# Optimization experiments

Measured on AMD Instinct MI355X. Metric: run time of the kernel, lower is better.

## Reference

```python
import jax, jax.numpy as jnp
import numpy as np

HEADS = 8
C_HEAD = 64  # head dim == in_dim of x
P0, P1 = 2, 3  # adaptive pool output


def setup_inputs() -> dict:
    key = jax.random.key(0)
    ks = jax.random.split(key, 8)
    b, c, h, w = 16, 64, 64, 96
    m, d = 6, 192
    inner = HEADS * C_HEAD  # 512
    return {
        "x": jax.random.normal(ks[0], (b, c, h, w), dtype=jnp.float32),
        "z": jax.random.normal(ks[1], (b, m, d), dtype=jnp.float32),
        "conv_w": jax.random.normal(ks[2], (192, c), dtype=jnp.float32) * 0.02,
        "conv_b": jax.random.normal(ks[3], (192,), dtype=jnp.float32) * 0.02,
        "wq": jax.random.normal(ks[4], (d, inner), dtype=jnp.float32) * 0.02,
        "bq": jax.random.normal(ks[5], (inner,), dtype=jnp.float32) * 0.02,
        "wo": jax.random.normal(ks[6], (inner, d), dtype=jnp.float32) * 0.02,
        "bo": jax.random.normal(ks[7], (d,), dtype=jnp.float32) * 0.02,
    }


def reference(x, z, conv_w, conv_b, wq, bq, wo, bo):
    b, c, h, w = x.shape
    _, m, d = z.shape
    # 1x1 conv (pointwise GEMM over channels) + bias
    xp = jnp.einsum('bchw,oc->bohw', x, conv_w) + conv_b[None, :, None, None]
    # AdaptiveAvgPool2d((2,3)) with exact divisibility -> block mean
    xp = xp.reshape(b, 192, P0, h // P0, P1, w // P1).mean(axis=(3, 5))  # [b,192,2,3]
    # view(b, d, m) then permute(0,2,1) -> [b, m, d]
    z = z + xp.reshape(b, d, m).transpose(0, 2, 1)
    # k = v: view(b, h*w, c), repeat heads along last dim, view(b, heads, h*w, c)
    # (row-major reshape reproduces torch .view semantics exactly)
    kv = jnp.tile(x.reshape(b, h * w, c), (1, 1, HEADS)).reshape(b, HEADS, h * w, C_HEAD)
    # q = Linear(dim, heads*c) then view(b, heads, m, c)
    q = (z @ wq + bq).reshape(b, HEADS, m, C_HEAD)
    scale = C_HEAD ** -0.5
    dots = jnp.einsum('bhmc,bhlc->bhml', q, kv) * scale  # [b,h,m,l]
    attn = jax.nn.softmax(dots, axis=-1)
    out = jnp.einsum('bhml,bhlc->bhmc', attn, kv)
    out = out.transpose(0, 2, 1, 3).reshape(b, m, HEADS * C_HEAD)  # b m (h c)
    return z + out @ wo + bo
```

## Files before the change

### kernel.cpp

```cpp
#include <hip/hip_runtime.h>

#define NB 16
#define NC 64
#define NM 6
#define ND 192
#define NHEADS 8
#define NCH 64
#define NINNER 512
#define PLANE 6144
#define XB (NC*PLANE)
#define NKEY 768
#define NCHUNK 8
#define CK 96

__global__ __launch_bounds__(256) void pool_kernel(const float* __restrict__ x,
                                                   float* __restrict__ xmean) {
    int bc = blockIdx.x;
    const float4* p = (const float4*)(x + (size_t)bc * PLANE);
    int tid = threadIdx.x;
    float acc[6] = {0.f,0.f,0.f,0.f,0.f,0.f};
    #pragma unroll
    for (int k = 0; k < 6; ++k) {
        int idx4 = tid + k * 256;
        int hh = idx4 / 24;
        int w4 = idx4 - hh * 24;
        int j = (hh >> 5) * 3 + (w4 >> 3);
        float4 v = p[idx4];
        acc[j] += v.x + v.y + v.z + v.w;
    }
    int lane = tid & 63, wave = tid >> 6;
    #pragma unroll
    for (int j = 0; j < 6; ++j) {
        float v = acc[j];
        for (int off = 32; off > 0; off >>= 1) v += __shfl_down(v, off, 64);
        acc[j] = v;
    }
    __shared__ float part[4][6];
    if (lane == 0) {
        #pragma unroll
        for (int j = 0; j < 6; ++j) part[wave][j] = acc[j];
    }
    __syncthreads();
    if (tid < 6) {
        float s = part[0][tid] + part[1][tid] + part[2][tid] + part[3][tid];
        xmean[bc * 6 + tid] = s * (1.0f / 1024.0f);
    }
}

__global__ __launch_bounds__(256) void zq_kernel(const float* __restrict__ z,
                                                 const float* __restrict__ conv_w,
                                                 const float* __restrict__ conv_b,
                                                 const float* __restrict__ wq,
                                                 const float* __restrict__ bq,
                                                 const float* __restrict__ xmean,
                                                 float* __restrict__ znew,
                                                 float* __restrict__ qr) {
    int blk = blockIdx.x;
    int cgrp = blk & 7, bm = blk >> 3;
    int b = bm / NM, m = bm - b * NM;
    int tid = threadIdx.x;
    __shared__ float xm[NC];
    __shared__ float zn[ND];
    __shared__ float qpart[3][64];
    if (tid < NC) xm[tid] = xmean[(b * NC + tid) * NM + m];
    __syncthreads();
    if (tid < ND) {
        float a = conv_b[tid];
        const float4* wr4 = (const float4*)(conv_w + tid * NC);
        #pragma unroll
        for (int c4 = 0; c4 < 16; ++c4) {
            float4 w = wr4[c4];
            a += w.x * xm[c4 * 4 + 0] + w.y * xm[c4 * 4 + 1]
               + w.z * xm[c4 * 4 + 2] + w.w * xm[c4 * 4 + 3];
        }
        float v = z[bm * ND + tid] + a;
        zn[tid] = v;
        if (cgrp == 0) znew[bm * ND + tid] = v;
    }
    __syncthreads();
    int colL = tid & 63, ks = tid >> 6;
    int col = cgrp * 64 + colL;
    float a = (ks == 0) ? bq[col] : 0.f;
    int d0 = ks * 48;
    #pragma unroll
    for (int d = d0; d < d0 + 48; ++d) a += zn[d] * wq[d * NINNER + col];
    if (ks > 0) qpart[ks - 1][colL] = a;
    __syncthreads();
    if (ks == 0) {
        float tot = a + qpart[0][colL] + qpart[1][colL] + qpart[2][colL];
        int t = m * 8 + cgrp;
        qr[b * (48 * 64) + t * 64 + colL] = tot;
    }
}

__global__ __launch_bounds__(256, 5) void fattn_kernel(const float* __restrict__ x,
                                                       const float* __restrict__ qr,
                                                       float* __restrict__ po,
                                                       float* __restrict__ ps) {
    int blk = blockIdx.x;
    int chunk = blk & 7, bh = blk >> 3;
    int head = bh & 7, b = bh >> 3;
    int tid = threadIdx.x;
    __shared__ float k_lds[CK][NCH];
    __shared__ float q_lds[NM][NCH];
    __shared__ float s_lds[NM][CK];
    const float* kbase = x + (size_t)b * XB + (size_t)(head * NKEY + chunk * CK) * NCH;

    for (int i = tid; i < NM * NCH; i += 256) {
        int mi = i >> 6, ch = i & 63;
        q_lds[mi][ch] = qr[b * (48 * 64) + (head * NM + mi) * 64 + ch];
    }
    const float4* k4 = (const float4*)kbase;
    #pragma unroll
    for (int r = 0; r < 6; ++r) {
        int i = tid + r * 256;
        int row = i >> 4, c4 = i & 15;
        float4 v = k4[i];
        *(float4*)&k_lds[row][c4 * 4] = v;
    }
    __syncthreads();

    if (tid < 96) {
        int u = tid;
        float a[NM] = {0.f,0.f,0.f,0.f,0.f,0.f};
        #pragma unroll
        for (int c4 = 0; c4 < 16; ++c4) {
            int cc = ((c4 + u) & 15) * 4;
            float4 kv = *(const float4*)&k_lds[u][cc];
            #pragma unroll
            for (int mo = 0; mo < NM; ++mo) {
                float4 qv = *(const float4*)&q_lds[mo][cc];
                a[mo] += kv.x*qv.x + kv.y*qv.y + kv.z*qv.z + kv.w*qv.w;
            }
        }
        #pragma unroll
        for (int mo = 0; mo < NM; ++mo) s_lds[mo][u] = __expf(a[mo] * 0.125f);
    }
    __syncthreads();

    int lane = tid & 63, wave = tid >> 6;

    if (wave < 2) {
        int ch = lane, m0 = wave * 3;
        float a0 = 0.f, a1 = 0.f, a2 = 0.f;
        #pragma unroll
        for (int u0 = 0; u0 < CK; u0 += 4) {
            float4 s0 = *(const float4*)&s_lds[m0 + 0][u0];
            float4 s1 = *(const float4*)&s_lds[m0 + 1][u0];
            float4 s2 = *(const float4*)&s_lds[m0 + 2][u0];
            float kv0 = k_lds[u0 + 0][ch];
            float kv1 = k_lds[u0 + 1][ch];
            float kv2 = k_lds[u0 + 2][ch];
            float kv3 = k_lds[u0 + 3][ch];
            a0 += s0.x*kv0 + s0.y*kv1 + s0.z*kv2 + s0.w*kv3;
            a1 += s1.x*kv0 + s1.y*kv1 + s1.z*kv2 + s1.w*kv3;
            a2 += s2.x*kv0 + s2.y*kv1 + s2.z*kv2 + s2.w*kv3;
        }
        float* pob = po + (size_t)blk * (NM * NCH);
        pob[(m0 + 0) * NCH + ch] = a0;
        pob[(m0 + 1) * NCH + ch] = a1;
        pob[(m0 + 2) * NCH + ch] = a2;
    } else {
        #pragma unroll
        for (int rnd = 0; rnd < 3; ++rnd) {
            int mi = rnd * 2 + (wave - 2);
            float v = s_lds[mi][lane] + ((lane < 32) ? s_lds[mi][64 + lane] : 0.f);
            for (int msk = 1; msk < 64; msk <<= 1) v += __shfl_xor(v, msk, 64);
            if (lane == 0) ps[blk * NM + mi] = v;
        }
    }
}

__global__ __launch_bounds__(256) void proj_kernel(const float* __restrict__ znew,
                                                   const float* __restrict__ po,
                                                   const float* __restrict__ ps,
                                                   const float* __restrict__ wo,
                                                   const float* __restrict__ bo,
                                                   float* __restrict__ out) {
    int blk = blockIdx.x;
    int cgrp = blk & 3, bm = blk >> 2;
    int b = bm / NM, m = bm - b * NM;
    int tid = threadIdx.x;
    __shared__ float4 orow4[128];
    __shared__ float4 part4[16][12];

    if (tid < 128) {
        int h = tid >> 4, c16 = tid & 15;
        int base = (b * NHEADS + h) * NCHUNK;
        const float4* po4 = (const float4*)po;
        float4 n = make_float4(0.f, 0.f, 0.f, 0.f);
        float den = 0.f;
        #pragma unroll
        for (int c = 0; c < NCHUNK; ++c) {
            float4 v = po4[(size_t)(base + c) * 96 + m * 16 + c16];
            n.x += v.x; n.y += v.y; n.z += v.z; n.w += v.w;
            den += ps[(base + c) * NM + m];
        }
        float inv = 1.0f / den;
        n.x *= inv; n.y *= inv; n.z *= inv; n.w *= inv;
        orow4[tid] = n;
    }
    __syncthreads();

    if (tid < 192) {
        int g4 = tid % 12, ks = tid / 12;
        int cb = cgrp * 12 + g4;
        const float4* wo4 = (const float4*)wo;
        const float* orow = (const float*)orow4;
        float4 acc = make_float4(0.f, 0.f, 0.f, 0.f);
        int i0 = ks * 32;
        #pragma unroll 8
        for (int i = i0; i < i0 + 32; ++i) {
            float s = orow[i];
            float4 w = wo4[i * 48 + cb];
            acc.x += s * w.x; acc.y += s * w.y; acc.z += s * w.z; acc.w += s * w.w;
        }
        part4[ks][g4] = acc;
    }
    __syncthreads();

    if (tid < 48) {
        int g4 = tid >> 2, j = tid & 3;
        float s = 0.f;
        #pragma unroll
        for (int ks = 0; ks < 16; ++ks) s += ((const float*)&part4[ks][g4])[j];
        int col = cgrp * 48 + tid;
        out[bm * ND + col] = s + bo[col] + znew[bm * ND + col];
    }
}

extern "C" void kernel_launch(void* const* d_in, const int* in_sizes, int n_in,
                              void* d_out, int out_size, void* d_ws, size_t ws_size,
                              hipStream_t stream) {
    const float* x      = (const float*)d_in[0];
    const float* z      = (const float*)d_in[1];
    const float* conv_w = (const float*)d_in[2];
    const float* conv_b = (const float*)d_in[3];
    const float* wq     = (const float*)d_in[4];
    const float* bq     = (const float*)d_in[5];
    const float* wo     = (const float*)d_in[6];
    const float* bo     = (const float*)d_in[7];
    float* out = (float*)d_out;

    float* ws    = (float*)d_ws;
    float* xmean = ws;
    float* znew  = ws + 6144;
    float* qr    = ws + 24576;
    float* po    = ws + 73728;
    float* ps    = ws + 466944;

    pool_kernel<<<NB*NC, 256, 0, stream>>>(x, xmean);
    zq_kernel<<<NB*NM*8, 256, 0, stream>>>(z, conv_w, conv_b, wq, bq, xmean, znew, qr);
    fattn_kernel<<<NB*NHEADS*NCHUNK, 256, 0, stream>>>(x, qr, po, ps);
    proj_kernel<<<NB*NM*4, 256, 0, stream>>>(znew, po, ps, wo, bo, out);
}
```

Measured before the change: 31.36 us.

## Split q projection algebraically so pooling and z-projection run in one launch

The q projection is split using linearity. The part from z+conv_b and the precomputed product conv_w^T·wq are computed in the same launch as the pooling, in independent block ranges. The remaining xmean·(conv_w^T wq) term is added inside the attention kernel, and proj recomputes znew from conv_w and xmean. This removes one kernel launch and the serial dependency between pooling and the q GEMM. In exchange, every attention block now does redundant 64-length dot products, and floating-point summation order changes.

```diff
diff --git a/kernel.cpp b/kernel.cpp
--- a/kernel.cpp
+++ b/kernel.cpp
@@ -13,90 +13,88 @@
 #define NCHUNK 8
 #define CK 96
 
-__global__ __launch_bounds__(256) void pool_kernel(const float* __restrict__ x,
-                                                   float* __restrict__ xmean) {
-    int bc = blockIdx.x;
-    const float4* p = (const float4*)(x + (size_t)bc * PLANE);
+__global__ __launch_bounds__(256) void k1_kernel(
+    const float* __restrict__ x, const float* __restrict__ z,
+    const float* __restrict__ conv_w, const float* __restrict__ conv_b,
+    const float* __restrict__ wq, const float* __restrict__ bq,
+    float* __restrict__ xmean, float* __restrict__ qz,
+    float* __restrict__ cwt)
+{
+    int bid = blockIdx.x;
     int tid = threadIdx.x;
-    float acc[6] = {0.f,0.f,0.f,0.f,0.f,0.f};
-    #pragma unroll
-    for (int k = 0; k < 6; ++k) {
-        int idx4 = tid + k * 256;
-        int hh = idx4 / 24;
-        int w4 = idx4 - hh * 24;
-        int j = (hh >> 5) * 3 + (w4 >> 3);
-        float4 v = p[idx4];
-        acc[j] += v.x + v.y + v.z + v.w;
-    }
-    int lane = tid & 63, wave = tid >> 6;
-    #pragma unroll
-    for (int j = 0; j < 6; ++j) {
-        float v = acc[j];
-        for (int off = 32; off > 0; off >>= 1) v += __shfl_down(v, off, 64);
-        acc[j] = v;
-    }
-    __shared__ float part[4][6];
-    if (lane == 0) {
-        #pragma unroll
-        for (int j = 0; j < 6; ++j) part[wave][j] = acc[j];
-    }
-    __syncthreads();
-    if (tid < 6) {
-        float s = part[0][tid] + part[1][tid] + part[2][tid] + part[3][tid];
-        xmean[bc * 6 + tid] = s * (1.0f / 1024.0f);
-    }
-}
-
-__global__ __launch_bounds__(256) void zq_kernel(const float* __restrict__ z,
-                                                 const float* __restrict__ conv_w,
-                                                 const float* __restrict__ conv_b,
-                                                 const float* __restrict__ wq,
-                                                 const float* __restrict__ bq,
-                                                 const float* __restrict__ xmean,
-                                                 float* __restrict__ znew,
-                                                 float* __restrict__ qr) {
-    int blk = blockIdx.x;
-    int cgrp = blk & 7, bm = blk >> 3;
-    int b = bm / NM, m = bm - b * NM;
-    int tid = threadIdx.x;
-    __shared__ float xm[NC];
-    __shared__ float zn[ND];
-    __shared__ float qpart[3][64];
-    if (tid < NC) xm[tid] = xmean[(b * NC + tid) * NM + m];
-    __syncthreads();
-    if (tid < ND) {
-        float a = conv_b[tid];
-        const float4* wr4 = (const float4*)(conv_w + tid * NC);
-        #pragma unroll
-        for (int c4 = 0; c4 < 16; ++c4) {
-            float4 w = wr4[c4];
-            a += w.x * xm[c4 * 4 + 0] + w.y * xm[c4 * 4 + 1]
-               + w.z * xm[c4 * 4 + 2] + w.w * xm[c4 * 4 + 3];
-        }
-        float v = z[bm * ND + tid] + a;
-        zn[tid] = v;
-        if (cgrp == 0) znew[bm * ND + tid] = v;
-    }
-    __syncthreads();
-    int colL = tid & 63, ks = tid >> 6;
-    int col = cgrp * 64 + colL;
-    float a = (ks == 0) ? bq[col] : 0.f;
-    int d0 = ks * 48;
-    #pragma unroll
-    for (int d = d0; d < d0 + 48; ++d) a += zn[d] * wq[d * NINNER + col];
-    if (ks > 0) qpart[ks - 1][colL] = a;
-    __syncthreads();
-    if (ks == 0) {
-        float tot = a + qpart[0][colL] + qpart[1][colL] + qpart[2][colL];
-        int t = m * 8 + cgrp;
-        qr[b * (48 * 64) + t * 64 + colL] = tot;
-    }
-}
-
-__global__ __launch_bounds__(256, 5) void fattn_kernel(const float* __restrict__ x,
-                                                       const float* __restrict__ qr,
-                                                       float* __restrict__ po,
-                                                       float* __restrict__ ps) {
+    __shared__ float sh[448];
+
+    if (bid < 1024) {
+        int bc = bid;
+        const float4* p = (const float4*)(x + (size_t)bc * PLANE);
+        float acc[6] = {0.f,0.f,0.f,0.f,0.f,0.f};
+        #pragma unroll
+        for (int k = 0; k < 6; ++k) {
+            int idx4 = tid + k * 256;
+            int hh = idx4 / 24;
+            int w4 = idx4 - hh * 24;
+            int j = (hh >> 5) * 3 + (w4 >> 3);
+            float4 v = p[idx4];
+            acc[j] += v.x + v.y + v.z + v.w;
+        }
+        int lane = tid & 63, wave = tid >> 6;
+        #pragma unroll
+        for (int j = 0; j < 6; ++j) {
+            float v = acc[j];
+            for (int off = 32; off > 0; off >>= 1) v += __shfl_down(v, off, 64);
+            acc[j] = v;
+        }
+        float* part = sh;
+        if (lane == 0) {
+            #pragma unroll
+            for (int j = 0; j < 6; ++j) part[wave * 6 + j] = acc[j];
+        }
+        __syncthreads();
+        if (tid < 6) {
+            float s = part[tid] + part[6 + tid] + part[12 + tid] + part[18 + tid];
+            xmean[bc * 6 + tid] = s * (1.0f / 1024.0f);
+        }
+    } else if (bid < 1792) {
+        int blk = bid - 1024;
+        int cgrp = blk & 7, bm = blk >> 3;
+        float* zc    = sh;
+        float* qpart = sh + 192;
+        if (tid < ND) zc[tid] = z[bm * ND + tid] + conv_b[tid];
+        __syncthreads();
+        int colL = tid & 63, ks = tid >> 6;
+        int col = cgrp * 64 + colL;
+        float a = (ks == 0) ? bq[col] : 0.f;
+        int d0 = ks * 48;
+        #pragma unroll
+        for (int d = d0; d < d0 + 48; ++d) a += zc[d] * wq[d * NINNER + col];
+        if (ks > 0) qpart[(ks - 1) * 64 + colL] = a;
+        __syncthreads();
+        if (ks == 0) {
+            qz[blk * 64 + colL] = a + qpart[colL] + qpart[64 + colL] + qpart[128 + colL];
+        }
+    } else {
+        int j = bid - 1792;
+        int c = tid & 63, cl0 = tid >> 6;
+        float a0 = 0.f, a1 = 0.f;
+        const float* wc = conv_w + c;
+        const float* w0 = wq + j * 8 + cl0;
+        const float* w1 = w0 + 4;
+        #pragma unroll 8
+        for (int d = 0; d < ND; ++d) {
+            float cwv = wc[d * NC];
+            a0 += cwv * w0[d * NINNER];
+            a1 += cwv * w1[d * NINNER];
+        }
+        cwt[(j * 8 + cl0    ) * 64 + c] = a0;
+        cwt[(j * 8 + cl0 + 4) * 64 + c] = a1;
+    }
+}
+
+__global__ __launch_bounds__(256, 5) void fattn_kernel(
+    const float* __restrict__ x, const float* __restrict__ qz,
+    const float* __restrict__ cwt, const float* __restrict__ xmean,
+    float* __restrict__ po, float* __restrict__ ps)
+{
     int blk = blockIdx.x;
     int chunk = blk & 7, bh = blk >> 3;
     int head = bh & 7, b = bh >> 3;
@@ -104,11 +102,12 @@
     __shared__ float k_lds[CK][NCH];
     __shared__ float q_lds[NM][NCH];
     __shared__ float s_lds[NM][CK];
+    __shared__ float xmT[NM][NC];
     const float* kbase = x + (size_t)b * XB + (size_t)(head * NKEY + chunk * CK) * NCH;
 
-    for (int i = tid; i < NM * NCH; i += 256) {
-        int mi = i >> 6, ch = i & 63;
-        q_lds[mi][ch] = qr[b * (48 * 64) + (head * NM + mi) * 64 + ch];
+    for (int i = tid; i < NC * NM; i += 256) {
+        int c = i / 6, m = i - c * 6;
+        xmT[m][c] = xmean[b * 384 + i];
     }
     const float4* k4 = (const float4*)kbase;
     #pragma unroll
@@ -117,6 +116,23 @@
         int row = i >> 4, c4 = i & 15;
         float4 v = k4[i];
         *(float4*)&k_lds[row][c4 * 4] = v;
+    }
+    __syncthreads();
+
+    for (int idx = tid; idx < NM * NCH; idx += 256) {
+        int mi = idx >> 6, ch = idx & 63;
+        int t = head * 6 + mi;
+        int mr = t >> 3;
+        int col = ((t & 7) << 6) | ch;
+        float a = qz[b * 3072 + t * 64 + ch];
+        const float4* cw4 = (const float4*)(cwt + col * 64);
+        const float4* xv4 = (const float4*)&xmT[mr][0];
+        #pragma unroll
+        for (int c4 = 0; c4 < 16; ++c4) {
+            float4 w = cw4[c4], v = xv4[c4];
+            a += w.x*v.x + w.y*v.y + w.z*v.z + w.w*v.w;
+        }
+        q_lds[mi][ch] = a;
     }
     __syncthreads();
 
@@ -139,7 +155,6 @@
     __syncthreads();
 
     int lane = tid & 63, wave = tid >> 6;
-
     if (wave < 2) {
         int ch = lane, m0 = wave * 3;
         float a0 = 0.f, a1 = 0.f, a2 = 0.f;
@@ -171,18 +186,22 @@
     }
 }
 
-__global__ __launch_bounds__(256) void proj_kernel(const float* __restrict__ znew,
-                                                   const float* __restrict__ po,
-                                                   const float* __restrict__ ps,
-                                                   const float* __restrict__ wo,
-                                                   const float* __restrict__ bo,
-                                                   float* __restrict__ out) {
+__global__ __launch_bounds__(256) void proj_kernel(
+    const float* __restrict__ z, const float* __restrict__ conv_w,
+    const float* __restrict__ conv_b, const float* __restrict__ xmean,
+    const float* __restrict__ po, const float* __restrict__ ps,
+    const float* __restrict__ wo, const float* __restrict__ bo,
+    float* __restrict__ out)
+{
     int blk = blockIdx.x;
     int cgrp = blk & 3, bm = blk >> 2;
     int b = bm / NM, m = bm - b * NM;
     int tid = threadIdx.x;
     __shared__ float4 orow4[128];
     __shared__ float4 part4[16][12];
+    __shared__ float xmc[NC];
+
+    if (tid < NC) xmc[tid] = xmean[b * 384 + tid * 6 + m];
 
     if (tid < 128) {
         int h = tid >> 4, c16 = tid & 15;
@@ -220,12 +239,20 @@
     __syncthreads();
 
     if (tid < 48) {
-        int g4 = tid >> 2, j = tid & 3;
+        int g4 = tid >> 2, jj = tid & 3;
         float s = 0.f;
         #pragma unroll
-        for (int ks = 0; ks < 16; ++ks) s += ((const float*)&part4[ks][g4])[j];
+        for (int ks = 0; ks < 16; ++ks) s += ((const float*)&part4[ks][g4])[jj];
         int col = cgrp * 48 + tid;
-        out[bm * ND + col] = s + bo[col] + znew[bm * ND + col];
+        float zn = z[bm * ND + col] + conv_b[col];
+        const float4* cw4 = (const float4*)(conv_w + col * NC);
+        const float4* xv4 = (const float4*)xmc;
+        #pragma unroll
+        for (int c4 = 0; c4 < 16; ++c4) {
+            float4 w = cw4[c4], v = xv4[c4];
+            zn += w.x*v.x + w.y*v.y + w.z*v.z + w.w*v.w;
+        }
+        out[bm * ND + col] = s + bo[col] + zn;
     }
 }
 
@@ -244,13 +271,14 @@
 
     float* ws    = (float*)d_ws;
     float* xmean = ws;
-    float* znew  = ws + 6144;
-    float* qr    = ws + 24576;
-    float* po    = ws + 73728;
-    float* ps    = ws + 466944;
-
-    pool_kernel<<<NB*NC, 256, 0, stream>>>(x, xmean);
-    zq_kernel<<<NB*NM*8, 256, 0, stream>>>(z, conv_w, conv_b, wq, bq, xmean, znew, qr);
-    fattn_kernel<<<NB*NHEADS*NCHUNK, 256, 0, stream>>>(x, qr, po, ps);
-    proj_kernel<<<NB*NM*4, 256, 0, stream>>>(znew, po, ps, wo, bo, out);
-}
+    float* qz    = ws + 6144;
+    float* cwt   = ws + 55296;
+    float* po    = ws + 88064;
+    float* ps    = ws + 481280;
+
+    k1_kernel<<<1856, 256, 0, stream>>>(x, z, conv_w, conv_b, wq, bq,
+                                        xmean, qz, cwt);
+    fattn_kernel<<<NB*NHEADS*NCHUNK, 256, 0, stream>>>(x, qz, cwt, xmean, po, ps);
+    proj_kernel<<<NB*NM*4, 256, 0, stream>>>(z, conv_w, conv_b, xmean,
+                                             po, ps, wo, bo, out);
+}
```

After: 44.84 us. 1.43x slower.
